# Kernel tuning notes

Hardware: AMD Instinct MI355X
Metric: run time of the kernel (lower is better)

The kernel has to match this reference:

```python
import jax, jax.numpy as jnp
import numpy as np
from jax import lax

C = 384          # input_dim
HEADS = 12       # num_heads_sp = max(1, 384*1.0 // 30)
HD = 32          # head_dim_sp = 384 // 12
NK = 3           # num_keys (full=True)
ATT_K, ATT_S = 7, 4
UP_K, UP_P = 8, 2   # ConvTranspose2d(kernel=att_stride*2, stride=4, padding=att_stride//2)
EPS = 1e-5
DN = ('NCHW', 'OIHW', 'NCHW')


def _gn(x, g, b):
    # GroupNorm(num_groups=1): normalize over (C,H,W) per sample, per-channel affine
    mu = jnp.mean(x, axis=(1, 2, 3), keepdims=True)
    var = jnp.var(x, axis=(1, 2, 3), keepdims=True)
    return (x - mu) * lax.rsqrt(var + EPS) * g[None, :, None, None] + b[None, :, None, None]


def _pw(x, w):
    # 1x1 conv as einsum; w: [out_ch, in_ch]
    return jnp.einsum('nchw,oc->nohw', x, w)


def _forward(x, dw_w, bn_gamma, bn_beta, bn_mean, bn_var, lnch_gamma, lnch_beta,
             pwise_ch_w, outch_w, outch_b, lnsp_gamma, lnsp_beta,
             pwise_sp_w, outsp_w, outsp_b, up_w, up_b):
    # depthwise strided downsampling conv + BatchNorm (eval mode)
    p = ATT_K // 2
    x_down = lax.conv_general_dilated(x, dw_w, (ATT_S, ATT_S), [(p, p), (p, p)],
                                      dimension_numbers=DN, feature_group_count=C)
    s = bn_gamma * lax.rsqrt(bn_var + EPS)
    x_down = x_down * s[None, :, None, None] + (bn_beta - bn_mean * s)[None, :, None, None]
    N, _, H, W = x_down.shape
    L = H * W
    # --- channel attention: tokens are channels, d_k = H*W ---
    qkv = _pw(_gn(x_down, lnch_gamma, lnch_beta), pwise_ch_w).reshape(N, NK * C, L)
    q, k, v = jnp.split(qkv, NK, axis=1)  # each [N, C, L]
    att = jax.nn.softmax(jnp.einsum('ncl,ndl->ncd', q, k) / jnp.sqrt(jnp.float32(L)), axis=-1)
    vals = jnp.einsum('ncd,ndl->ncl', att, v).reshape(N, C, H, W)
    x_down = x_down + _pw(vals, outch_w) + outch_b[None, :, None, None]
    # --- spatial multi-head attention over the H*W tokens ---
    qkv = _pw(_gn(x_down, lnsp_gamma, lnsp_beta), pwise_sp_w)
    qkv = qkv.reshape(N, HEADS, NK * HD, L).transpose(0, 1, 3, 2)  # [N,h,L,3*hd]
    q, k, v = jnp.split(qkv, NK, axis=-1)  # each [N,h,L,hd]
    att = jax.nn.softmax(jnp.einsum('nhld,nhmd->nhlm', q, k) / jnp.sqrt(jnp.float32(HD)), axis=-1)
    vals = jnp.einsum('nhlm,nhmd->nhld', att, v).transpose(0, 1, 3, 2).reshape(N, HEADS * HD, H, W)
    x_down = x_down + _pw(vals, outsp_w) + outsp_b[None, :, None, None]
    # --- depthwise transposed-conv upsampling (as lhs-dilated conv w/ flipped kernel) ---
    tp = UP_K - 1 - UP_P
    o = lax.conv_general_dilated(x_down, up_w[:, :, ::-1, ::-1], (1, 1), [(tp, tp), (tp, tp)],
                                 lhs_dilation=(ATT_S, ATT_S), dimension_numbers=DN,
                                 feature_group_count=C)
    return x + o + up_b[None, :, None, None]


def setup_inputs():
    key = jax.random.key(0)
    ks = jax.random.split(key, 8)
    w = lambda k, shp: jax.random.normal(k, shp, dtype=jnp.float32) * 0.05
    return {
        'x': jax.random.normal(ks[0], (16, C, 64, 64), dtype=jnp.float32),
        'dw_w': w(ks[1], (C, 1, ATT_K, ATT_K)),
        'bn_gamma': jnp.ones((C,), jnp.float32),
        'bn_beta': jnp.zeros((C,), jnp.float32),
        'bn_mean': jnp.zeros((C,), jnp.float32),
        'bn_var': jnp.ones((C,), jnp.float32),
        'lnch_gamma': jnp.ones((C,), jnp.float32),
        'lnch_beta': jnp.zeros((C,), jnp.float32),
        'pwise_ch_w': w(ks[2], (NK * C, C)),
        'outch_w': w(ks[3], (C, C)),
        'outch_b': jnp.zeros((C,), jnp.float32),
        'lnsp_gamma': jnp.ones((C,), jnp.float32),
        'lnsp_beta': jnp.zeros((C,), jnp.float32),
        'pwise_sp_w': w(ks[4], (NK * HEADS * HD, C)),
        'outsp_w': w(ks[5], (C, HEADS * HD)),
        'outsp_b': jnp.zeros((C,), jnp.float32),
        'up_w': w(ks[6], (C, 1, UP_K, UP_K)),
        'up_b': jnp.zeros((C,), jnp.float32),
    }


def reference(x, dw_w, bn_gamma, bn_beta, bn_mean, bn_var, lnch_gamma, lnch_beta,
              pwise_ch_w, outch_w, outch_b, lnsp_gamma, lnsp_beta,
              pwise_sp_w, outsp_w, outsp_b, up_w, up_b):
    return _forward(x, dw_w, bn_gamma, bn_beta, bn_mean, bn_var, lnch_gamma, lnch_beta,
                    pwise_ch_w, outch_w, outch_b, lnsp_gamma, lnsp_beta,
                    pwise_sp_w, outsp_w, outsp_b, up_w, up_b)
```

## Files before the change

kernel.cpp:

```cpp
#include <hip/hip_runtime.h>
#include <hip/hip_bf16.h>
#include <math.h>

typedef __hip_bfloat16 bf16;

#define NB  16
#define CCH 384
#define LDIM 256

typedef __attribute__((ext_vector_type(8))) short bh8;
typedef __attribute__((ext_vector_type(4))) float fx4;

__device__ __forceinline__ float ldin(const void* p, long i, bool f) {
    if (f) return ((const float*)p)[i];
    return __bfloat162float(((const bf16*)p)[i]);
}
__device__ __forceinline__ float b2f(unsigned short u) {
    union { unsigned short s; bf16 b; } c; c.s = u; return __bfloat162float(c.b);
}
__device__ __forceinline__ unsigned short f2b(float v) {
    bf16 h = __float2bfloat16(v);
    union { bf16 b; unsigned short s; } c; c.b = h; return c.s;
}
__device__ __forceinline__ float fin(float v, float marker) {
    return (v == v && fabsf(v) < 1e30f) ? v : marker;
}

__global__ void k_detect(const unsigned* __restrict__ g, int* __restrict__ flag) {
    if (threadIdx.x == 0) *flag = (*g == 0x3F800000u) ? 1 : 0;
}
__global__ void k_zero(float* __restrict__ p) { p[threadIdx.x] = 0.f; }

__global__ void k_dwconv_bn(const void* __restrict__ x, const void* __restrict__ w,
                            const void* __restrict__ gamma, const void* __restrict__ beta,
                            const void* __restrict__ mean, const void* __restrict__ var,
                            const int* __restrict__ flag, float* __restrict__ xd)
{
    bool f = *flag != 0;
    int c = blockIdx.x, n = blockIdx.y, t = threadIdx.x;
    int i = t >> 4, j = t & 15;
    float s = ldin(gamma, c, f) * rsqrtf(ldin(var, c, f) + 1e-5f);
    float bias = ldin(beta, c, f) - ldin(mean, c, f) * s;
    long xbase = (long)(n * CCH + c) << 12;
    float acc = 0.f;
    #pragma unroll
    for (int a = 0; a < 7; a++) {
        int yy = 4 * i + a - 3;
        if (yy < 0 || yy >= 64) continue;
        #pragma unroll
        for (int b = 0; b < 7; b++) {
            int xx = 4 * j + b - 3;
            if (xx < 0 || xx >= 64) continue;
            acc += ldin(x, xbase + (yy << 6) + xx, f) * ldin(w, c * 49 + a * 7 + b, f);
        }
    }
    xd[((long)(n * CCH + c) << 8) + t] = fin(acc * s + bias, 1.0e4f);
}

__global__ void k_gn_stats(const float* __restrict__ xd, float* __restrict__ stats)
{
    int n = blockIdx.y;
    const float* p = xd + (long)n * (CCH * LDIM) + blockIdx.x * 4096;
    float s = 0.f, s2 = 0.f;
    for (int i = threadIdx.x; i < 4096; i += 256) {
        float v = p[i];
        s += v; s2 += v * v;
    }
    #pragma unroll
    for (int o = 32; o; o >>= 1) { s += __shfl_down(s, o); s2 += __shfl_down(s2, o); }
    __shared__ float sh[4], sh2[4];
    int wid = threadIdx.x >> 6, lane = threadIdx.x & 63;
    if (lane == 0) { sh[wid] = s; sh2[wid] = s2; }
    __syncthreads();
    if (threadIdx.x == 0) {
        atomicAdd(&stats[n * 2],     sh[0] + sh[1] + sh[2] + sh[3]);
        atomicAdd(&stats[n * 2 + 1], sh2[0] + sh2[1] + sh2[2] + sh2[3]);
    }
}

template<bool TB, bool ACCUM, bool AIN, bool GNB>
__global__ __launch_bounds__(256) void k_gemm(
    const void* __restrict__ A, const float* __restrict__ B, float* __restrict__ Cm,
    const void* __restrict__ bias, const int* __restrict__ flag,
    const float* __restrict__ gnstats, const void* __restrict__ gng, const void* __restrict__ gnbt,
    int M, int N, int K, int lda, int ldb, int ldc, long sA, long sB, long sC, float alpha)
{
    bool f = *flag != 0;
    __shared__ unsigned short As[128 * 40];
    __shared__ unsigned short Bs[128 * 40];
    long aoff = (long)blockIdx.z * sA;
    const float* Bb = B + (long)blockIdx.z * sB;
    float* Cb = Cm + (long)blockIdx.z * sC;
    float mu = 0.f, rs = 0.f;
    if (GNB) {
        float S = gnstats[2 * blockIdx.z], S2 = gnstats[2 * blockIdx.z + 1];
        mu = S * (1.f / 98304.f);
        float var = S2 * (1.f / 98304.f) - mu * mu;
        rs = rsqrtf(fmaxf(var, 0.f) + 1e-5f);
    }
    int m0 = blockIdx.y << 7, n0 = blockIdx.x << 7;
    int t = threadIdx.x;
    int w = t >> 6, lane = t & 63;
    int wm = w >> 1, wn = w & 1;
    int lr = lane & 15, lg = lane >> 4;
    int amloc = t >> 3, akloc = (t & 7) << 2;
    int nloc = t & 127, ph = t >> 7;
    fx4 acc[4][4] = {};

    for (int k0 = 0; k0 < K; k0 += 32) {
        #pragma unroll
        for (int p = 0; p < 4; p++) {
            int m = (p << 5) + amloc;
            long ai = aoff + (long)(m0 + m) * lda + k0 + akloc;
            ushort4 uv;
            if (AIN && !f) {
                uv = *(const ushort4*)((const unsigned short*)A + ai);
            } else {
                float4 fv = *(const float4*)((const float*)A + ai);
                uv.x = f2b(fv.x); uv.y = f2b(fv.y); uv.z = f2b(fv.z); uv.w = f2b(fv.w);
            }
            *(ushort4*)&As[m * 40 + akloc] = uv;
        }
        if (!TB) {
            const float* Bp = Bb + n0 + nloc;
            #pragma unroll
            for (int i = 0; i < 8; i++) {
                int p = ph + (i << 1);
                int k = k0 + (p << 1);
                float v0 = Bp[(long)k * ldb];
                float v1 = Bp[(long)(k + 1) * ldb];
                if (GNB) {
                    v0 = (v0 - mu) * rs * ldin(gng, k, f) + ldin(gnbt, k, f);
                    v1 = (v1 - mu) * rs * ldin(gng, k + 1, f) + ldin(gnbt, k + 1, f);
                }
                unsigned int pk = (unsigned)f2b(v0) | ((unsigned)f2b(v1) << 16);
                *(unsigned int*)&Bs[nloc * 40 + (p << 1)] = pk;
            }
        } else {
            #pragma unroll
            for (int p = 0; p < 4; p++) {
                int n = (p << 5) + amloc;
                float4 fv = *(const float4*)(Bb + (long)(n0 + n) * ldb + k0 + akloc);
                ushort4 uv;
                uv.x = f2b(fv.x); uv.y = f2b(fv.y); uv.z = f2b(fv.z); uv.w = f2b(fv.w);
                *(ushort4*)&Bs[n * 40 + akloc] = uv;
            }
        }
        __syncthreads();
        bh8 a[4], b[4];
        #pragma unroll
        for (int mi = 0; mi < 4; mi++)
            a[mi] = *(const bh8*)&As[((wm << 6) + (mi << 4) + lr) * 40 + (lg << 3)];
        #pragma unroll
        for (int nj = 0; nj < 4; nj++)
            b[nj] = *(const bh8*)&Bs[((wn << 6) + (nj << 4) + lr) * 40 + (lg << 3)];
        #pragma unroll
        for (int mi = 0; mi < 4; mi++)
            #pragma unroll
            for (int nj = 0; nj < 4; nj++)
                acc[mi][nj] = __builtin_amdgcn_mfma_f32_16x16x32_bf16(a[mi], b[nj], acc[mi][nj], 0, 0, 0);
        __syncthreads();
    }
    #pragma unroll
    for (int mi = 0; mi < 4; mi++) {
        #pragma unroll
        for (int r = 0; r < 4; r++) {
            int m = m0 + (wm << 6) + (mi << 4) + (lg << 2) + r;
            float bv = bias ? ldin(bias, m, f) : 0.f;
            #pragma unroll
            for (int nj = 0; nj < 4; nj++) {
                int n = n0 + (wn << 6) + (nj << 4) + lr;
                long idx = (long)m * ldc + n;
                float v = alpha * acc[mi][nj][r] + bv;
                if (ACCUM) v += Cb[idx];
                Cb[idx] = fin(v, 4.0e4f);
            }
        }
    }
}

__global__ void k_softmax(float* __restrict__ a, int D)
{
    long row = blockIdx.x;
    float* p = a + row * D;
    int t = threadIdx.x;
    float m = -1e30f;
    for (int i = t; i < D; i += 256) m = fmaxf(m, p[i]);
    #pragma unroll
    for (int o = 32; o; o >>= 1) m = fmaxf(m, __shfl_down(m, o));
    __shared__ float shm[4], shs[4];
    int wid = t >> 6, lane = t & 63;
    if (lane == 0) shm[wid] = m;
    __syncthreads();
    m = fmaxf(fmaxf(shm[0], shm[1]), fmaxf(shm[2], shm[3]));
    float s = 0.f;
    for (int i = t; i < D; i += 256) {
        float e = __expf(p[i] - m);
        p[i] = e;
        s += e;
    }
    #pragma unroll
    for (int o = 32; o; o >>= 1) s += __shfl_down(s, o);
    if (lane == 0) shs[wid] = s;
    __syncthreads();
    float inv = 1.f / (shs[0] + shs[1] + shs[2] + shs[3]);
    for (int i = t; i < D; i += 256) p[i] *= inv;
}

__global__ __launch_bounds__(256, 1) void k_spatt(const float* __restrict__ qkv,
                                                  float* __restrict__ vals)
{
    __shared__ __align__(16) unsigned char smem[152064];
    unsigned short* Qs = (unsigned short*)smem;
    unsigned short* Ks = (unsigned short*)(smem + 20480);
    unsigned char*  Ps = smem;
    unsigned char*  Vs = smem + 135168;
    float*          Os = (float*)smem;

    int h = blockIdx.x, n = blockIdx.y, t = threadIdx.x;
    const float* base = qkv + (long)n * 294912 + h * 96 * 256;

    {
        const float* q0 = base + t;
        const float* k0 = base + 32 * 256 + t;
        #pragma unroll
        for (int dp = 0; dp < 16; dp++) {
            float a0 = q0[(2 * dp) * 256], a1 = q0[(2 * dp + 1) * 256];
            ((unsigned*)Qs)[t * 20 + dp] = (unsigned)f2b(a0) | ((unsigned)f2b(a1) << 16);
            float b0 = k0[(2 * dp) * 256], b1 = k0[(2 * dp + 1) * 256];
            ((unsigned*)Ks)[t * 20 + dp] = (unsigned)f2b(b0) | ((unsigned)f2b(b1) << 16);
        }
    }
    {
        int d = t >> 3, tok0 = (t & 7) << 5;
        const float* vp = base + (64 + d) * 256 + tok0;
        int swz = (d & 7) << 4;
        #pragma unroll
        for (int i = 0; i < 8; i++) {
            float4 fv = *(const float4*)(vp + 4 * i);
            ushort4 uv;
            uv.x = f2b(fv.x); uv.y = f2b(fv.y); uv.z = f2b(fv.z); uv.w = f2b(fv.w);
            *(ushort4*)(Vs + d * 528 + ((((tok0 + 4 * i) * 2)) ^ swz)) = uv;
        }
    }
    __syncthreads();

    int lane = t & 63;
    int lr = lane & 15, lg = lane >> 4;
    int rbase = (t >> 6) << 6;

    fx4 acc[4][16] = {};
    {
        bh8 a[4];
        #pragma unroll
        for (int mi = 0; mi < 4; mi++)
            a[mi] = *(const bh8*)&Qs[(rbase + mi * 16 + lr) * 40 + lg * 8];
        #pragma unroll
        for (int nj = 0; nj < 16; nj++) {
            bh8 b = *(const bh8*)&Ks[(nj * 16 + lr) * 40 + lg * 8];
            #pragma unroll
            for (int mi = 0; mi < 4; mi++)
                acc[mi][nj] = __builtin_amdgcn_mfma_f32_16x16x32_bf16(a[mi], b, acc[mi][nj], 0, 0, 0);
        }
    }
    __syncthreads();

    float inv[4][4];
    const float scl = 0.17677669529663687f;
    #pragma unroll
    for (int mi = 0; mi < 4; mi++) {
        #pragma unroll
        for (int r = 0; r < 4; r++) {
            float s[16];
            float mx = -1e30f;
            #pragma unroll
            for (int nj = 0; nj < 16; nj++) { s[nj] = acc[mi][nj][r] * scl; mx = fmaxf(mx, s[nj]); }
            #pragma unroll
            for (int o = 8; o; o >>= 1) mx = fmaxf(mx, __shfl_xor(mx, o));
            int row = rbase + mi * 16 + lg * 4 + r;
            int swz = (row & 7) << 4;
            unsigned char* prow = Ps + row * 528;
            float sum = 0.f;
            #pragma unroll
            for (int nj = 0; nj < 16; nj++) {
                float p = __expf(s[nj] - mx);
                sum += p;
                int col = nj * 16 + lr;
                *(unsigned short*)(prow + ((col * 2) ^ swz)) = f2b(p);
            }
            #pragma unroll
            for (int o = 8; o; o >>= 1) sum += __shfl_xor(sum, o);
            inv[mi][r] = 1.f / sum;
        }
    }

    fx4 acc2[4][2] = {};
    #pragma unroll
    for (int ks = 0; ks < 8; ks++) {
        bh8 pa[4], vb[2];
        #pragma unroll
        for (int mi = 0; mi < 4; mi++) {
            int row = rbase + mi * 16 + lr;
            pa[mi] = *(const bh8*)(Ps + row * 528 + ((ks * 64 + lg * 16) ^ ((row & 7) << 4)));
        }
        #pragma unroll
        for (int nj = 0; nj < 2; nj++) {
            int row = nj * 16 + lr;
            vb[nj] = *(const bh8*)(Vs + row * 528 + ((ks * 64 + lg * 16) ^ ((row & 7) << 4)));
        }
        #pragma unroll
        for (int mi = 0; mi < 4; mi++)
            #pragma unroll
            for (int nj = 0; nj < 2; nj++)
                acc2[mi][nj] = __builtin_amdgcn_mfma_f32_16x16x32_bf16(pa[mi], vb[nj], acc2[mi][nj], 0, 0, 0);
    }
    __syncthreads();

    #pragma unroll
    for (int mi = 0; mi < 4; mi++)
        #pragma unroll
        for (int nj = 0; nj < 2; nj++)
            #pragma unroll
            for (int r = 0; r < 4; r++) {
                int tok = rbase + mi * 16 + lg * 4 + r;
                int d = nj * 16 + lr;
                Os[d * 265 + tok] = acc2[mi][nj][r] * inv[mi][r];
            }
    __syncthreads();

    long ob = (long)n * 98304 + (long)h * 8192;
    #pragma unroll
    for (int d = 0; d < 32; d++)
        vals[ob + d * 256 + t] = fin(Os[d * 265 + t], 5.0e4f);
}

__global__ void k_upsample(const void* __restrict__ x, const float* __restrict__ xd,
                           const void* __restrict__ w, const void* __restrict__ ub,
                           const int* __restrict__ flag, void* __restrict__ out)
{
    bool f = *flag != 0;
    int c = blockIdx.y, n = blockIdx.z;
    int t = threadIdx.x;
    int p0 = (blockIdx.x * 256 + t) * 4;
    int y = p0 >> 6, xx0 = p0 & 63;
    const float* xdp = xd + ((long)(n * CCH + c) << 8);
    long base = (long)(n * CCH + c) << 12;
    float bias = ldin(ub, c, f);
    float acc[4];
    if (f) {
        #pragma unroll
        for (int e = 0; e < 4; e++) acc[e] = ((const float*)x)[base + p0 + e] + bias;
    } else {
        ushort4 xv = *(const ushort4*)((const unsigned short*)x + base + p0);
        acc[0] = b2f(xv.x) + bias; acc[1] = b2f(xv.y) + bias;
        acc[2] = b2f(xv.z) + bias; acc[3] = b2f(xv.w) + bias;
    }
    int ry = (y + 2) & 3;
    #pragma unroll
    for (int dy = 0; dy < 2; dy++) {
        int ky = ry + 4 * dy;
        int iy = (y + 2 - ky) >> 2;
        if (iy < 0 || iy >= 16) continue;
        #pragma unroll
        for (int e = 0; e < 4; e++) {
            int xxe = xx0 + e;
            int rx = (xxe + 2) & 3;
            #pragma unroll
            for (int dx = 0; dx < 2; dx++) {
                int kx = rx + 4 * dx;
                int ix = (xxe + 2 - kx) >> 2;
                if (ix < 0 || ix >= 16) continue;
                acc[e] += xdp[(iy << 4) + ix] * ldin(w, (c << 6) + (ky << 3) + kx, f);
            }
        }
    }
    if (f) {
        #pragma unroll
        for (int e = 0; e < 4; e++) ((float*)out)[base + p0 + e] = fin(acc[e], 9.0e4f);
    } else {
        ushort4 ov;
        ov.x = f2b(fin(acc[0], 9.0e4f)); ov.y = f2b(fin(acc[1], 9.0e4f));
        ov.z = f2b(fin(acc[2], 9.0e4f)); ov.w = f2b(fin(acc[3], 9.0e4f));
        *(ushort4*)((unsigned short*)out + base + p0) = ov;
    }
}

extern "C" void kernel_launch(void* const* d_in, const int* in_sizes, int n_in,
                              void* d_out, int out_size, void* d_ws, size_t ws_size,
                              hipStream_t stream)
{
    const void* x       = d_in[0];
    const void* dw_w    = d_in[1];
    const void* bn_g    = d_in[2];
    const void* bn_b    = d_in[3];
    const void* bn_m    = d_in[4];
    const void* bn_v    = d_in[5];
    const void* lnch_g  = d_in[6];
    const void* lnch_b  = d_in[7];
    const void* w_ch    = d_in[8];
    const void* outch_w = d_in[9];
    const void* outch_b = d_in[10];
    const void* lnsp_g  = d_in[11];
    const void* lnsp_b  = d_in[12];
    const void* w_sp    = d_in[13];
    const void* outsp_w = d_in[14];
    const void* outsp_b = d_in[15];
    const void* up_w    = d_in[16];
    const void* up_b    = d_in[17];
    float* ws = (float*)d_ws;

    float* xd    = ws;
    float* stats = ws + 1572864;
    int*   flag  = (int*)(ws + 1572864 + 32);

    float* ob   = (float*)d_out;
    float* vals = ob;
    float* qkv  = ob + 1572864;
    float* attb = qkv + 4718592;

    k_detect<<<1, 64, 0, stream>>>((const unsigned*)bn_g, flag);

    k_dwconv_bn<<<dim3(CCH, NB), 256, 0, stream>>>(x, dw_w, bn_g, bn_b, bn_m, bn_v, flag, xd);
    k_zero<<<1, 32, 0, stream>>>(stats);
    k_gn_stats<<<dim3(24, NB), 256, 0, stream>>>(xd, stats);
    k_gemm<false, false, true, true><<<dim3(2, 9, NB), 256, 0, stream>>>(
        w_ch, xd, qkv, nullptr, flag, stats, lnch_g, lnch_b,
        1152, 256, 384, 384, 256, 256, 0L, 98304L, 294912L, 1.f);
    k_gemm<true, false, false, false><<<dim3(3, 3, NB), 256, 0, stream>>>(
        qkv, qkv + 98304, attb, nullptr, flag, nullptr, nullptr, nullptr,
        384, 384, 256, 256, 256, 384, 294912L, 294912L, 147456L, 0.0625f);
    k_softmax<<<NB * 384, 256, 0, stream>>>(attb, 384);
    k_gemm<false, false, false, false><<<dim3(2, 3, NB), 256, 0, stream>>>(
        attb, qkv + 196608, vals, nullptr, flag, nullptr, nullptr, nullptr,
        384, 256, 384, 384, 256, 256, 147456L, 294912L, 98304L, 1.f);
    k_gemm<false, true, true, false><<<dim3(2, 3, NB), 256, 0, stream>>>(
        outch_w, vals, xd, outch_b, flag, nullptr, nullptr, nullptr,
        384, 256, 384, 384, 256, 256, 0L, 98304L, 98304L, 1.f);
    k_zero<<<1, 32, 0, stream>>>(stats);
    k_gn_stats<<<dim3(24, NB), 256, 0, stream>>>(xd, stats);
    k_gemm<false, false, true, true><<<dim3(2, 9, NB), 256, 0, stream>>>(
        w_sp, xd, qkv, nullptr, flag, stats, lnsp_g, lnsp_b,
        1152, 256, 384, 384, 256, 256, 0L, 98304L, 294912L, 1.f);
    k_spatt<<<dim3(12, NB), 256, 0, stream>>>(qkv, vals);
    k_gemm<false, true, true, false><<<dim3(2, 3, NB), 256, 0, stream>>>(
        outsp_w, vals, xd, outsp_b, flag, nullptr, nullptr, nullptr,
        384, 256, 384, 384, 256, 256, 0L, 98304L, 98304L, 1.f);
    k_upsample<<<dim3(4, CCH, NB), 256, 0, stream>>>(x, xd, up_w, up_b, flag, d_out);
}
```

Before: 582.8 us.

## Fuse GroupNorm statistics into dwconv and out-projection GEMM; tile dwconv input in LDS

The depthwise conv now stages each 64x64 input plane into zero-padded shared memory with vectorized loads, keeps the 7x7 weights in registers, and reads padded rows as float4 instead of doing bounds-checked scalar global loads. It also reduces per-block sum and sum-of-squares and adds them atomically into the GroupNorm stats. The channel-attention output GEMM gains a STAT template path that accumulates the second GroupNorm's statistics in its epilogue. Together these remove both k_gn_stats launches and one k_zero, avoiding two extra passes over xd. The cost is more shared memory per dwconv block and atomics from many blocks.

```diff
diff --git a/kernel.cpp b/kernel.cpp
--- a/kernel.cpp
+++ b/kernel.cpp
@@ -31,58 +31,87 @@
 }
 __global__ void k_zero(float* __restrict__ p) { p[threadIdx.x] = 0.f; }
 
-__global__ void k_dwconv_bn(const void* __restrict__ x, const void* __restrict__ w,
+__global__ __launch_bounds__(256) void k_dwconv_bn(const void* __restrict__ x, const void* __restrict__ w,
                             const void* __restrict__ gamma, const void* __restrict__ beta,
                             const void* __restrict__ mean, const void* __restrict__ var,
-                            const int* __restrict__ flag, float* __restrict__ xd)
+                            const int* __restrict__ flag, float* __restrict__ xd,
+                            float* __restrict__ stats)
 {
     bool f = *flag != 0;
+    __shared__ __align__(16) float xs[68 * 76];
     int c = blockIdx.x, n = blockIdx.y, t = threadIdx.x;
-    int i = t >> 4, j = t & 15;
+
+    #pragma unroll
+    for (int z = 0; z < 6; z++) {
+        int idx = t + (z << 8);
+        if (idx < 1292) ((float4*)xs)[idx] = (float4){0.f, 0.f, 0.f, 0.f};
+    }
+
+    float W[7][7];
+    #pragma unroll
+    for (int a = 0; a < 7; a++)
+        #pragma unroll
+        for (int b = 0; b < 7; b++) W[a][b] = ldin(w, c * 49 + a * 7 + b, f);
     float s = ldin(gamma, c, f) * rsqrtf(ldin(var, c, f) + 1e-5f);
     float bias = ldin(beta, c, f) - ldin(mean, c, f) * s;
+    __syncthreads();
+
     long xbase = (long)(n * CCH + c) << 12;
+    {
+        int row = t >> 2, col0 = (t & 3) << 4;
+        float* dst = &xs[(row + 4) * 76 + col0 + 4];
+        if (f) {
+            const float* xp = (const float*)x + xbase + (row << 6) + col0;
+            #pragma unroll
+            for (int i2 = 0; i2 < 4; i2++) ((float4*)dst)[i2] = ((const float4*)xp)[i2];
+        } else {
+            const unsigned short* xp = (const unsigned short*)x + xbase + (row << 6) + col0;
+            #pragma unroll
+            for (int i2 = 0; i2 < 2; i2++) {
+                bh8 v8 = *(const bh8*)(xp + (i2 << 3));
+                float4 f0 = { b2f((unsigned short)v8[0]), b2f((unsigned short)v8[1]),
+                              b2f((unsigned short)v8[2]), b2f((unsigned short)v8[3]) };
+                float4 f1 = { b2f((unsigned short)v8[4]), b2f((unsigned short)v8[5]),
+                              b2f((unsigned short)v8[6]), b2f((unsigned short)v8[7]) };
+                ((float4*)dst)[i2 * 2]     = f0;
+                ((float4*)dst)[i2 * 2 + 1] = f1;
+            }
+        }
+    }
+    __syncthreads();
+
+    int i = t >> 4, j = t & 15;
     float acc = 0.f;
     #pragma unroll
     for (int a = 0; a < 7; a++) {
-        int yy = 4 * i + a - 3;
-        if (yy < 0 || yy >= 64) continue;
-        #pragma unroll
-        for (int b = 0; b < 7; b++) {
-            int xx = 4 * j + b - 3;
-            if (xx < 0 || xx >= 64) continue;
-            acc += ldin(x, xbase + (yy << 6) + xx, f) * ldin(w, c * 49 + a * 7 + b, f);
-        }
-    }
-    xd[((long)(n * CCH + c) << 8) + t] = fin(acc * s + bias, 1.0e4f);
-}
-
-__global__ void k_gn_stats(const float* __restrict__ xd, float* __restrict__ stats)
-{
-    int n = blockIdx.y;
-    const float* p = xd + (long)n * (CCH * LDIM) + blockIdx.x * 4096;
-    float s = 0.f, s2 = 0.f;
-    for (int i = threadIdx.x; i < 4096; i += 256) {
-        float v = p[i];
-        s += v; s2 += v * v;
-    }
-    #pragma unroll
-    for (int o = 32; o; o >>= 1) { s += __shfl_down(s, o); s2 += __shfl_down(s2, o); }
-    __shared__ float sh[4], sh2[4];
-    int wid = threadIdx.x >> 6, lane = threadIdx.x & 63;
-    if (lane == 0) { sh[wid] = s; sh2[wid] = s2; }
-    __syncthreads();
-    if (threadIdx.x == 0) {
-        atomicAdd(&stats[n * 2],     sh[0] + sh[1] + sh[2] + sh[3]);
-        atomicAdd(&stats[n * 2 + 1], sh2[0] + sh2[1] + sh2[2] + sh2[3]);
-    }
-}
-
-template<bool TB, bool ACCUM, bool AIN, bool GNB>
+        const float* rp = &xs[(4 * i + a + 1) * 76 + (j << 2)];
+        float4 lo = *(const float4*)rp;
+        float4 hi = *(const float4*)(rp + 4);
+        acc += lo.y * W[a][0] + lo.z * W[a][1] + lo.w * W[a][2] + hi.x * W[a][3]
+             + hi.y * W[a][4] + hi.z * W[a][5] + hi.w * W[a][6];
+    }
+    float v = fin(acc * s + bias, 1.0e4f);
+    xd[((long)(n * CCH + c) << 8) + t] = v;
+
+    float s1 = v, s2 = v * v;
+    #pragma unroll
+    for (int o = 32; o; o >>= 1) { s1 += __shfl_down(s1, o); s2 += __shfl_down(s2, o); }
+    __shared__ float sa[4], sb[4];
+    int wid = t >> 6, ln = t & 63;
+    if (ln == 0) { sa[wid] = s1; sb[wid] = s2; }
+    __syncthreads();
+    if (t == 0) {
+        atomicAdd(&stats[n * 2],     sa[0] + sa[1] + sa[2] + sa[3]);
+        atomicAdd(&stats[n * 2 + 1], sb[0] + sb[1] + sb[2] + sb[3]);
+    }
+}
+
+template<bool TB, bool ACCUM, bool AIN, bool GNB, bool STAT>
 __global__ __launch_bounds__(256) void k_gemm(
     const void* __restrict__ A, const float* __restrict__ B, float* __restrict__ Cm,
     const void* __restrict__ bias, const int* __restrict__ flag,
     const float* __restrict__ gnstats, const void* __restrict__ gng, const void* __restrict__ gnbt,
+    float* __restrict__ gnout,
     int M, int N, int K, int lda, int ldb, int ldc, long sA, long sB, long sC, float alpha)
 {
     bool f = *flag != 0;
@@ -161,6 +190,7 @@
                 acc[mi][nj] = __builtin_amdgcn_mfma_f32_16x16x32_bf16(a[mi], b[nj], acc[mi][nj], 0, 0, 0);
         __syncthreads();
     }
+    float s1 = 0.f, s2 = 0.f;
     #pragma unroll
     for (int mi = 0; mi < 4; mi++) {
         #pragma unroll
@@ -173,8 +203,22 @@
                 long idx = (long)m * ldc + n;
                 float v = alpha * acc[mi][nj][r] + bv;
                 if (ACCUM) v += Cb[idx];
-                Cb[idx] = fin(v, 4.0e4f);
-            }
+                v = fin(v, 4.0e4f);
+                Cb[idx] = v;
+                if (STAT) { s1 += v; s2 += v * v; }
+            }
+        }
+    }
+    if (STAT) {
+        #pragma unroll
+        for (int o = 32; o; o >>= 1) { s1 += __shfl_down(s1, o); s2 += __shfl_down(s2, o); }
+        __shared__ float sa[4], sb[4];
+        int wid = t >> 6, ln2 = t & 63;
+        if (ln2 == 0) { sa[wid] = s1; sb[wid] = s2; }
+        __syncthreads();
+        if (t == 0) {
+            atomicAdd(&gnout[2 * blockIdx.z],     sa[0] + sa[1] + sa[2] + sa[3]);
+            atomicAdd(&gnout[2 * blockIdx.z + 1], sb[0] + sb[1] + sb[2] + sb[3]);
         }
     }
 }
@@ -411,7 +455,7 @@
 
     float* xd    = ws;
     float* stats = ws + 1572864;
-    int*   flag  = (int*)(ws + 1572864 + 32);
+    int*   flag  = (int*)(ws + 1572864 + 64);
 
     float* ob   = (float*)d_out;
     float* vals = ob;
@@ -419,31 +463,28 @@
     float* attb = qkv + 4718592;
 
     k_detect<<<1, 64, 0, stream>>>((const unsigned*)bn_g, flag);
-
-    k_dwconv_bn<<<dim3(CCH, NB), 256, 0, stream>>>(x, dw_w, bn_g, bn_b, bn_m, bn_v, flag, xd);
-    k_zero<<<1, 32, 0, stream>>>(stats);
-    k_gn_stats<<<dim3(24, NB), 256, 0, stream>>>(xd, stats);
-    k_gemm<false, false, true, true><<<dim3(2, 9, NB), 256, 0, stream>>>(
-        w_ch, xd, qkv, nullptr, flag, stats, lnch_g, lnch_b,
+    k_zero<<<1, 64, 0, stream>>>(stats);
+
+    k_dwconv_bn<<<dim3(CCH, NB), 256, 0, stream>>>(x, dw_w, bn_g, bn_b, bn_m, bn_v, flag, xd, stats);
+    k_gemm<false, false, true, true, false><<<dim3(2, 9, NB), 256, 0, stream>>>(
+        w_ch, xd, qkv, nullptr, flag, stats, lnch_g, lnch_b, nullptr,
         1152, 256, 384, 384, 256, 256, 0L, 98304L, 294912L, 1.f);
-    k_gemm<true, false, false, false><<<dim3(3, 3, NB), 256, 0, stream>>>(
-        qkv, qkv + 98304, attb, nullptr, flag, nullptr, nullptr, nullptr,
+    k_gemm<true, false, false, false, false><<<dim3(3, 3, NB), 256, 0, stream>>>(
+        qkv, qkv + 98304, attb, nullptr, flag, nullptr, nullptr, nullptr, nullptr,
         384, 384, 256, 256, 256, 384, 294912L, 294912L, 147456L, 0.0625f);
     k_softmax<<<NB * 384, 256, 0, stream>>>(attb, 384);
-    k_gemm<false, false, false, false><<<dim3(2, 3, NB), 256, 0, stream>>>(
-        attb, qkv + 196608, vals, nullptr, flag, nullptr, nullptr, nullptr,
+    k_gemm<false, false, false, false, false><<<dim3(2, 3, NB), 256, 0, stream>>>(
+        attb, qkv + 196608, vals, nullptr, flag, nullptr, nullptr, nullptr, nullptr,
         384, 256, 384, 384, 256, 256, 147456L, 294912L, 98304L, 1.f);
-    k_gemm<false, true, true, false><<<dim3(2, 3, NB), 256, 0, stream>>>(
-        outch_w, vals, xd, outch_b, flag, nullptr, nullptr, nullptr,
+    k_gemm<false, true, true, false, true><<<dim3(2, 3, NB), 256, 0, stream>>>(
+        outch_w, vals, xd, outch_b, flag, nullptr, nullptr, nullptr, stats + 32,
         384, 256, 384, 384, 256, 256, 0L, 98304L, 98304L, 1.f);
-    k_zero<<<1, 32, 0, stream>>>(stats);
-    k_gn_stats<<<dim3(24, NB), 256, 0, stream>>>(xd, stats);
-    k_gemm<false, false, true, true><<<dim3(2, 9, NB), 256, 0, stream>>>(
-        w_sp, xd, qkv, nullptr, flag, stats, lnsp_g, lnsp_b,
+    k_gemm<false, false, true, true, false><<<dim3(2, 9, NB), 256, 0, stream>>>(
+        w_sp, xd, qkv, nullptr, flag, stats + 32, lnsp_g, lnsp_b, nullptr,
         1152, 256, 384, 384, 256, 256, 0L, 98304L, 294912L, 1.f);
     k_spatt<<<dim3(12, NB), 256, 0, stream>>>(qkv, vals);
-    k_gemm<false, true, true, false><<<dim3(2, 3, NB), 256, 0, stream>>>(
-        outsp_w, vals, xd, outsp_b, flag, nullptr, nullptr, nullptr,
+    k_gemm<false, true, true, false, false><<<dim3(2, 3, NB), 256, 0, stream>>>(
+        outsp_w, vals, xd, outsp_b, flag, nullptr, nullptr, nullptr, nullptr,
         384, 256, 384, 384, 256, 256, 0L, 98304L, 98304L, 1.f);
     k_upsample<<<dim3(4, CCH, NB), 256, 0, stream>>>(x, xd, up_w, up_b, flag, d_out);
 }
```

Result: slower. 639.3 us (+9.7%).

## Fuse GroupNorm statistics into producer kernels via per-block partial sums

Applied to the files above, without the earlier changes.

Removes the separate zero and GroupNorm-statistics kernels. The dwconv kernel and the out-projection GEMM epilogue now write per-wave or per-block partial sums and sums of squares, and the consuming GEMM reduces those partials at block start. This saves two launches and one re-read of xd per GroupNorm, and drops the atomics. In exchange every QKV GEMM block redundantly reduces up to 1536 partials, and the partial buffers live inside the output buffer.

```diff
diff --git a/kernel.cpp b/kernel.cpp
--- a/kernel.cpp
+++ b/kernel.cpp
@@ -29,12 +29,12 @@
 __global__ void k_detect(const unsigned* __restrict__ g, int* __restrict__ flag) {
     if (threadIdx.x == 0) *flag = (*g == 0x3F800000u) ? 1 : 0;
 }
-__global__ void k_zero(float* __restrict__ p) { p[threadIdx.x] = 0.f; }
 
 __global__ void k_dwconv_bn(const void* __restrict__ x, const void* __restrict__ w,
                             const void* __restrict__ gamma, const void* __restrict__ beta,
                             const void* __restrict__ mean, const void* __restrict__ var,
-                            const int* __restrict__ flag, float* __restrict__ xd)
+                            const int* __restrict__ flag, float* __restrict__ xd,
+                            float* __restrict__ part)
 {
     bool f = *flag != 0;
     int c = blockIdx.x, n = blockIdx.y, t = threadIdx.x;
@@ -54,35 +54,25 @@
             acc += ldin(x, xbase + (yy << 6) + xx, f) * ldin(w, c * 49 + a * 7 + b, f);
         }
     }
-    xd[((long)(n * CCH + c) << 8) + t] = fin(acc * s + bias, 1.0e4f);
-}
-
-__global__ void k_gn_stats(const float* __restrict__ xd, float* __restrict__ stats)
-{
-    int n = blockIdx.y;
-    const float* p = xd + (long)n * (CCH * LDIM) + blockIdx.x * 4096;
-    float s = 0.f, s2 = 0.f;
-    for (int i = threadIdx.x; i < 4096; i += 256) {
-        float v = p[i];
-        s += v; s2 += v * v;
-    }
-    #pragma unroll
-    for (int o = 32; o; o >>= 1) { s += __shfl_down(s, o); s2 += __shfl_down(s2, o); }
-    __shared__ float sh[4], sh2[4];
-    int wid = threadIdx.x >> 6, lane = threadIdx.x & 63;
-    if (lane == 0) { sh[wid] = s; sh2[wid] = s2; }
-    __syncthreads();
-    if (threadIdx.x == 0) {
-        atomicAdd(&stats[n * 2],     sh[0] + sh[1] + sh[2] + sh[3]);
-        atomicAdd(&stats[n * 2 + 1], sh2[0] + sh2[1] + sh2[2] + sh2[3]);
-    }
-}
-
-template<bool TB, bool ACCUM, bool AIN, bool GNB>
+    float v = fin(acc * s + bias, 1.0e4f);
+    xd[((long)(n * CCH + c) << 8) + t] = v;
+
+    float s1 = v, s2 = v * v;
+    #pragma unroll
+    for (int o = 32; o; o >>= 1) { s1 += __shfl_down(s1, o); s2 += __shfl_down(s2, o); }
+    if ((t & 63) == 0) {
+        long slot = ((long)(n * CCH + c) << 2) + (t >> 6);
+        part[slot * 2]     = s1;
+        part[slot * 2 + 1] = s2;
+    }
+}
+
+template<bool TB, bool ACCUM, bool AIN, bool GNB, bool STAT>
 __global__ __launch_bounds__(256) void k_gemm(
     const void* __restrict__ A, const float* __restrict__ B, float* __restrict__ Cm,
     const void* __restrict__ bias, const int* __restrict__ flag,
     const float* __restrict__ gnstats, const void* __restrict__ gng, const void* __restrict__ gnbt,
+    float* __restrict__ gnout, int gncount,
     int M, int N, int K, int lda, int ldb, int ldc, long sA, long sB, long sC, float alpha)
 {
     bool f = *flag != 0;
@@ -91,15 +81,24 @@
     long aoff = (long)blockIdx.z * sA;
     const float* Bb = B + (long)blockIdx.z * sB;
     float* Cb = Cm + (long)blockIdx.z * sC;
+    int t = threadIdx.x;
     float mu = 0.f, rs = 0.f;
     if (GNB) {
-        float S = gnstats[2 * blockIdx.z], S2 = gnstats[2 * blockIdx.z + 1];
+        const float2* pp = (const float2*)(gnstats + (long)blockIdx.z * (gncount << 1));
+        float l1 = 0.f, l2 = 0.f;
+        for (int i2 = t; i2 < gncount; i2 += 256) { float2 pv = pp[i2]; l1 += pv.x; l2 += pv.y; }
+        #pragma unroll
+        for (int o = 32; o; o >>= 1) { l1 += __shfl_down(l1, o); l2 += __shfl_down(l2, o); }
+        __shared__ float r1[4], r2[4];
+        if ((t & 63) == 0) { r1[t >> 6] = l1; r2[t >> 6] = l2; }
+        __syncthreads();
+        float S  = r1[0] + r1[1] + r1[2] + r1[3];
+        float S2 = r2[0] + r2[1] + r2[2] + r2[3];
         mu = S * (1.f / 98304.f);
         float var = S2 * (1.f / 98304.f) - mu * mu;
         rs = rsqrtf(fmaxf(var, 0.f) + 1e-5f);
     }
     int m0 = blockIdx.y << 7, n0 = blockIdx.x << 7;
-    int t = threadIdx.x;
     int w = t >> 6, lane = t & 63;
     int wm = w >> 1, wn = w & 1;
     int lr = lane & 15, lg = lane >> 4;
@@ -161,6 +160,7 @@
                 acc[mi][nj] = __builtin_amdgcn_mfma_f32_16x16x32_bf16(a[mi], b[nj], acc[mi][nj], 0, 0, 0);
         __syncthreads();
     }
+    float s1 = 0.f, s2 = 0.f;
     #pragma unroll
     for (int mi = 0; mi < 4; mi++) {
         #pragma unroll
@@ -173,8 +173,24 @@
                 long idx = (long)m * ldc + n;
                 float v = alpha * acc[mi][nj][r] + bv;
                 if (ACCUM) v += Cb[idx];
-                Cb[idx] = fin(v, 4.0e4f);
-            }
+                v = fin(v, 4.0e4f);
+                Cb[idx] = v;
+                if (STAT) { s1 += v; s2 += v * v; }
+            }
+        }
+    }
+    if (STAT) {
+        #pragma unroll
+        for (int o = 32; o; o >>= 1) { s1 += __shfl_down(s1, o); s2 += __shfl_down(s2, o); }
+        __shared__ float sa[4], sb[4];
+        int wid = t >> 6;
+        if ((t & 63) == 0) { sa[wid] = s1; sb[wid] = s2; }
+        __syncthreads();
+        if (t == 0) {
+            int nblk = gridDim.x * gridDim.y;
+            int slot = blockIdx.z * nblk + blockIdx.y * gridDim.x + blockIdx.x;
+            gnout[slot * 2]     = sa[0] + sa[1] + sa[2] + sa[3];
+            gnout[slot * 2 + 1] = sb[0] + sb[1] + sb[2] + sb[3];
         }
     }
 }
@@ -410,40 +426,37 @@
     float* ws = (float*)d_ws;
 
     float* xd    = ws;
-    float* stats = ws + 1572864;
-    int*   flag  = (int*)(ws + 1572864 + 32);
-
-    float* ob   = (float*)d_out;
-    float* vals = ob;
-    float* qkv  = ob + 1572864;
-    float* attb = qkv + 4718592;
+    int*   flag  = (int*)(ws + 1572864);
+
+    float* ob    = (float*)d_out;
+    float* vals  = ob;
+    float* qkv   = ob + 1572864;
+    float* attb  = qkv + 4718592;
+    float* part1 = ob + 9437184;
+    float* part2 = part1 + 49152;
 
     k_detect<<<1, 64, 0, stream>>>((const unsigned*)bn_g, flag);
 
-    k_dwconv_bn<<<dim3(CCH, NB), 256, 0, stream>>>(x, dw_w, bn_g, bn_b, bn_m, bn_v, flag, xd);
-    k_zero<<<1, 32, 0, stream>>>(stats);
-    k_gn_stats<<<dim3(24, NB), 256, 0, stream>>>(xd, stats);
-    k_gemm<false, false, true, true><<<dim3(2, 9, NB), 256, 0, stream>>>(
-        w_ch, xd, qkv, nullptr, flag, stats, lnch_g, lnch_b,
+    k_dwconv_bn<<<dim3(CCH, NB), 256, 0, stream>>>(x, dw_w, bn_g, bn_b, bn_m, bn_v, flag, xd, part1);
+    k_gemm<false, false, true, true, false><<<dim3(2, 9, NB), 256, 0, stream>>>(
+        w_ch, xd, qkv, nullptr, flag, part1, lnch_g, lnch_b, nullptr, 1536,
         1152, 256, 384, 384, 256, 256, 0L, 98304L, 294912L, 1.f);
-    k_gemm<true, false, false, false><<<dim3(3, 3, NB), 256, 0, stream>>>(
-        qkv, qkv + 98304, attb, nullptr, flag, nullptr, nullptr, nullptr,
+    k_gemm<true, false, false, false, false><<<dim3(3, 3, NB), 256, 0, stream>>>(
+        qkv, qkv + 98304, attb, nullptr, flag, nullptr, nullptr, nullptr, nullptr, 0,
         384, 384, 256, 256, 256, 384, 294912L, 294912L, 147456L, 0.0625f);
     k_softmax<<<NB * 384, 256, 0, stream>>>(attb, 384);
-    k_gemm<false, false, false, false><<<dim3(2, 3, NB), 256, 0, stream>>>(
-        attb, qkv + 196608, vals, nullptr, flag, nullptr, nullptr, nullptr,
+    k_gemm<false, false, false, false, false><<<dim3(2, 3, NB), 256, 0, stream>>>(
+        attb, qkv + 196608, vals, nullptr, flag, nullptr, nullptr, nullptr, nullptr, 0,
         384, 256, 384, 384, 256, 256, 147456L, 294912L, 98304L, 1.f);
-    k_gemm<false, true, true, false><<<dim3(2, 3, NB), 256, 0, stream>>>(
-        outch_w, vals, xd, outch_b, flag, nullptr, nullptr, nullptr,
+    k_gemm<false, true, true, false, true><<<dim3(2, 3, NB), 256, 0, stream>>>(
+        outch_w, vals, xd, outch_b, flag, nullptr, nullptr, nullptr, part2, 0,
         384, 256, 384, 384, 256, 256, 0L, 98304L, 98304L, 1.f);
-    k_zero<<<1, 32, 0, stream>>>(stats);
-    k_gn_stats<<<dim3(24, NB), 256, 0, stream>>>(xd, stats);
-    k_gemm<false, false, true, true><<<dim3(2, 9, NB), 256, 0, stream>>>(
-        w_sp, xd, qkv, nullptr, flag, stats, lnsp_g, lnsp_b,
+    k_gemm<false, false, true, true, false><<<dim3(2, 9, NB), 256, 0, stream>>>(
+        w_sp, xd, qkv, nullptr, flag, part2, lnsp_g, lnsp_b, nullptr, 6,
         1152, 256, 384, 384, 256, 256, 0L, 98304L, 294912L, 1.f);
     k_spatt<<<dim3(12, NB), 256, 0, stream>>>(qkv, vals);
-    k_gemm<false, true, true, false><<<dim3(2, 3, NB), 256, 0, stream>>>(
-        outsp_w, vals, xd, outsp_b, flag, nullptr, nullptr, nullptr,
+    k_gemm<false, true, true, false, false><<<dim3(2, 3, NB), 256, 0, stream>>>(
+        outsp_w, vals, xd, outsp_b, flag, nullptr, nullptr, nullptr, nullptr, 0,
         384, 256, 384, 384, 256, 256, 0L, 98304L, 98304L, 1.f);
     k_upsample<<<dim3(4, CCH, NB), 256, 0, stream>>>(x, xd, up_w, up_b, flag, d_out);
 }
```

Measured after the change: 563.7 us. 1.03x faster.
